# Kernel optimization log

Hardware: AMD Instinct MI355X
Metric: run time of the kernel (lower is better)

Reference implementation:

```python
import jax, jax.numpy as jnp
import numpy as np

B, T, D = 4, 2048, 1024
H = 16
HD = D // H  # 64
MAX_POS = 4096


def setup_inputs() -> dict:
    key = jax.random.key(0)
    k1, k2, k3, k4 = jax.random.split(key, 4)
    x = jax.random.normal(k1, (B, T, D), dtype=jnp.float32)
    position_ids = jnp.sort(jax.random.randint(k2, (B, T), 0, MAX_POS), axis=-1)
    Wqkv = jax.random.normal(k3, (D, 3 * D), dtype=jnp.float32) * (D ** -0.5)
    Wout = jax.random.normal(k4, (D, D), dtype=jnp.float32) * (D ** -0.5)
    return {"x": x, "position_ids": position_ids, "Wqkv": Wqkv, "Wout": Wout}


def reference(x, position_ids, Wqkv, Wout):
    Bv, Tv, Dv = x.shape
    # qkv projection: (B,T,3,H,HD)
    qkv = (x @ Wqkv).reshape(Bv, Tv, 3, H, HD)
    q, k, v = jnp.moveaxis(qkv, 2, 0)  # each (B,T,H,HD)
    q = q.transpose(0, 2, 1, 3)  # (B,H,T,HD)
    k = k.transpose(0, 2, 1, 3)
    v = v.transpose(0, 2, 1, 3)
    scale = 1.0 / jnp.sqrt(jnp.asarray(HD, dtype=x.dtype))
    attn = jnp.einsum('bhid,bhjd->bhij', q, k) * scale  # (B,H,T,T)
    # position-derived causal mask: attend only where pos_i >= pos_j
    causal_mask = position_ids[:, None, :, None] < position_ids[:, None, None, :]
    attn = jnp.where(causal_mask, -jnp.inf, attn)
    attn = jax.nn.softmax(attn, axis=-1)
    attn = jnp.nan_to_num(attn, nan=0.0)
    out = jnp.einsum('bhij,bhjd->bhid', attn, v)  # (B,H,T,HD)
    out = out.transpose(0, 2, 1, 3).reshape(Bv, Tv, Dv)
    return out @ Wout
```

## Files before the change

kernel.cpp:

```cpp
#include <hip/hip_runtime.h>
#include <math.h>

#define NB 4
#define NT 2048
#define ND 1024
#define NH 16
#define NHD 64
#define N3D 3072
#define M1 8192

typedef __attribute__((ext_vector_type(8))) short bf16x8;
typedef __attribute__((ext_vector_type(4))) float f32x4;
typedef __attribute__((ext_vector_type(16))) float f32x16;
typedef __attribute__((ext_vector_type(2))) int i32x2;
typedef unsigned short u16;
typedef unsigned int u32;

#define MNEG -3.0e38f

__device__ __forceinline__ u32 bf16rn(float f) {
    u32 u = __float_as_uint(f);
    return (u + 0x7FFFu + ((u >> 16) & 1u)) >> 16;
}
__device__ __forceinline__ u32 pack2(float a, float b) {
    return bf16rn(a) | (bf16rn(b) << 16);
}
__device__ __forceinline__ u32 cvtpk(float lo, float hi) {
    u32 r;
    asm("v_cvt_pk_bf16_f32 %0, %1, %2" : "=v"(r) : "v"(lo), "v"(hi));
    return r;
}
__device__ __forceinline__ void pswap(u32& a, u32& b) {
    i32x2 r = __builtin_amdgcn_permlane32_swap((int)a, (int)b, false, false);
    a = (u32)r.x; b = (u32)r.y;
}

__global__ __launch_bounds__(256) void bnd_kernel(const int* __restrict__ pos, int* __restrict__ Bnd) {
    const int row = blockIdx.x * 256 + threadIdx.x;
    const int b = row >> 11, i = row & 2047;
    const int target = pos[b * 2048 + i];
    int lo = 0, hi = 2048;
    #pragma unroll
    for (int it = 0; it < 12; ++it) {
        const int mid = (lo + hi) >> 1;
        if (lo < hi) { if (pos[b * 2048 + mid] <= target) lo = mid + 1; else hi = mid; }
    }
    Bnd[row] = lo;
}

__global__ __launch_bounds__(256) void convx_kernel(const float* __restrict__ in, u16* __restrict__ out) {
    const int idx = blockIdx.x * 256 + threadIdx.x;
    const float4 v = *reinterpret_cast<const float4*>(in + (size_t)idx * 4);
    *reinterpret_cast<uint2*>(out + (size_t)idx * 4) = make_uint2(pack2(v.x, v.y), pack2(v.z, v.w));
}

__global__ __launch_bounds__(256) void tconv_kernel(const float* __restrict__ in, u16* __restrict__ out,
                                                    int R, int C) {
    __shared__ float t[32][33];
    const int bx = blockIdx.x * 32, by = blockIdx.y * 32;
    const int x = threadIdx.x, y0 = threadIdx.y;
    #pragma unroll
    for (int yy = y0; yy < 32; yy += 8) t[yy][x] = in[(size_t)(by + yy) * C + bx + x];
    __syncthreads();
    #pragma unroll
    for (int yy = y0; yy < 32; yy += 8) out[(size_t)(bx + yy) * R + by + x] = (u16)bf16rn(t[x][yy]);
}

#define GEMM_PROLOGUE(Aptr, Btptr)                                                            \
    __shared__ __align__(16) u16 As[4096];                                                    \
    __shared__ __align__(16) u16 Bs[4096];                                                    \
    const int tid = threadIdx.x;                                                              \
    const int lane = tid & 63, wave = tid >> 6;                                               \
    const int wr = wave >> 1, wc = wave & 1;                                                  \
    const int n0 = blockIdx.x * 128, m0 = blockIdx.y * 128;                                   \
    const int c0 = tid, c1 = tid + 256;                                                      \
    const int pA0 = (c0 * 16) ^ ((((c0 * 16) >> 6) & 7) << 4);                                \
    const int pA1 = (c1 * 16) ^ ((((c1 * 16) >> 6) & 7) << 4);                                \
    const u16* gA0 = Aptr + (size_t)(m0 + (c0 >> 2)) * 1024 + (c0 & 3) * 8;                   \
    const u16* gA1 = Aptr + (size_t)(m0 + (c1 >> 2)) * 1024 + (c1 & 3) * 8;                   \
    const u16* gB0 = Btptr + (size_t)(n0 + (c0 >> 2)) * 1024 + (c0 & 3) * 8;                  \
    const u16* gB1 = Btptr + (size_t)(n0 + (c1 >> 2)) * 1024 + (c1 & 3) * 8;                  \
    int offA[4], offB[4];                                                                     \
    {                                                                                         \
        const int kb = (lane >> 4) * 16;                                                      \
        _Pragma("unroll")                                                                     \
        for (int mm = 0; mm < 4; ++mm) {                                                      \
            int row = wr * 64 + mm * 16 + (lane & 15);                                        \
            offA[mm] = (row * 64 + kb) ^ ((row & 7) << 4);                                    \
        }                                                                                     \
        _Pragma("unroll")                                                                     \
        for (int nn = 0; nn < 4; ++nn) {                                                      \
            int row = wc * 64 + nn * 16 + (lane & 15);                                        \
            offB[nn] = (row * 64 + kb) ^ ((row & 7) << 4);                                    \
        }                                                                                     \
    }                                                                                         \
    f32x4 acc[4][4];                                                                          \
    _Pragma("unroll")                                                                         \
    for (int mm = 0; mm < 4; ++mm)                                                            \
        _Pragma("unroll")                                                                     \
        for (int nn = 0; nn < 4; ++nn)                                                        \
            acc[mm][nn] = (f32x4){0.f, 0.f, 0.f, 0.f};                                        \
    uint4 va0 = *(const uint4*)gA0, va1 = *(const uint4*)gA1;                                 \
    uint4 vb0 = *(const uint4*)gB0, vb1 = *(const uint4*)gB1;                                 \
    for (int k0 = 0; k0 < 1024; k0 += 32) {                                                   \
        __syncthreads();                                                                      \
        *(uint4*)((char*)As + pA0) = va0;                                                     \
        *(uint4*)((char*)As + pA1) = va1;                                                     \
        *(uint4*)((char*)Bs + pA0) = vb0;                                                     \
        *(uint4*)((char*)Bs + pA1) = vb1;                                                     \
        __syncthreads();                                                                      \
        if (k0 + 32 < 1024) {                                                                 \
            gA0 += 32; gA1 += 32; gB0 += 32; gB1 += 32;                                       \
            va0 = *(const uint4*)gA0; va1 = *(const uint4*)gA1;                               \
            vb0 = *(const uint4*)gB0; vb1 = *(const uint4*)gB1;                               \
        }                                                                                     \
        bf16x8 aF[4], bF[4];                                                                  \
        _Pragma("unroll")                                                                     \
        for (int mm = 0; mm < 4; ++mm) aF[mm] = *(const bf16x8*)((const char*)As + offA[mm]); \
        _Pragma("unroll")                                                                     \
        for (int nn = 0; nn < 4; ++nn) bF[nn] = *(const bf16x8*)((const char*)Bs + offB[nn]); \
        _Pragma("unroll")                                                                     \
        for (int mm = 0; mm < 4; ++mm)                                                        \
            _Pragma("unroll")                                                                 \
            for (int nn = 0; nn < 4; ++nn)                                                    \
                acc[mm][nn] = __builtin_amdgcn_mfma_f32_16x16x32_bf16(bF[nn], aF[mm],         \
                                                                      acc[mm][nn], 0, 0, 0); \
    }

__global__ __launch_bounds__(256) void gemm_qkv_kernel(
    const u16* __restrict__ A, const u16* __restrict__ Bt,
    u16* __restrict__ Qo, u16* __restrict__ Ko, u16* __restrict__ Vo)
{
    GEMM_PROLOGUE(A, Bt)
    const int col16 = lane & 15, g4 = (lane >> 4) << 2;
    const int nb0 = n0 + wc * 64;
    const int tb0 = m0 + wr * 64;
    const int s  = nb0 >> 10;
    const int hh = (nb0 >> 6) & 15;
    const int t0g = tb0 & 2047;
    const int bh = ((tb0 >> 11) << 4) + hh;
    const float sc = (s == 0) ? 0.18033688011112042f : 1.0f;

    __syncthreads();
    u16* lds = (wave & 1) ? Bs : As;
    for (int round = 0; round < 2; ++round) {
        if ((wave >> 1) == round) {
            if (s < 2) {
                #pragma unroll
                for (int mm = 0; mm < 4; ++mm) {
                    const int tl = mm * 16 + col16;
                    #pragma unroll
                    for (int nn = 0; nn < 4; ++nn) {
                        uint2 w = make_uint2(pack2(acc[mm][nn][0] * sc, acc[mm][nn][1] * sc),
                                             pack2(acc[mm][nn][2] * sc, acc[mm][nn][3] * sc));
                        const int off = (tl * 128 + (nn * 16 + g4) * 2) ^ ((tl & 7) << 4);
                        *reinterpret_cast<uint2*>((char*)lds + off) = w;
                    }
                }
                u16* dst = (s == 0) ? Qo : Ko;
                #pragma unroll
                for (int it = 0; it < 8; ++it) {
                    const int row = it * 8 + (lane >> 3);
                    const int off = (row * 128 + (lane & 7) * 16) ^ ((row & 7) << 4);
                    uint4 v = *reinterpret_cast<const uint4*>((const char*)lds + off);
                    *reinterpret_cast<uint4*>(&dst[((size_t)bh * 2048 + t0g + row) * 64 + (lane & 7) * 8]) = v;
                }
            } else {
                #pragma unroll
                for (int mm = 0; mm < 4; ++mm) {
                    const int tl = mm * 16 + col16;
                    #pragma unroll
                    for (int nn = 0; nn < 4; ++nn) {
                        #pragma unroll
                        for (int r = 0; r < 4; ++r) {
                            const int dl = nn * 16 + g4 + r;
                            const int off = (dl * 128 + tl * 2) ^ ((dl & 7) << 4);
                            *reinterpret_cast<u16*>((char*)lds + off) = (u16)bf16rn(acc[mm][nn][r]);
                        }
                    }
                }
                #pragma unroll
                for (int it = 0; it < 8; ++it) {
                    const int row = it * 8 + (lane >> 3);
                    const int off = (row * 128 + (lane & 7) * 16) ^ ((row & 7) << 4);
                    uint4 v = *reinterpret_cast<const uint4*>((const char*)lds + off);
                    *reinterpret_cast<uint4*>(&Vo[((size_t)bh * 64 + row) * 2048 + t0g + (lane & 7) * 8]) = v;
                }
            }
        }
        __syncthreads();
    }
}

__global__ __launch_bounds__(256) void gemm_out_kernel(
    const u16* __restrict__ A, const u16* __restrict__ Bt, float* __restrict__ C)
{
    GEMM_PROLOGUE(A, Bt)
    const int col16 = lane & 15, g4 = (lane >> 4) << 2;
    __syncthreads();
    char* lds = (char*)((wave & 1) ? Bs : As);
    for (int round = 0; round < 2; ++round) {
        if ((wave >> 1) == round) {
            #pragma unroll
            for (int p = 0; p < 2; ++p) {
                #pragma unroll
                for (int mmh = 0; mmh < 2; ++mmh) {
                    const int mm = p * 2 + mmh;
                    const int rl = mmh * 16 + col16;
                    #pragma unroll
                    for (int nn = 0; nn < 4; ++nn) {
                        const int off = (rl * 256 + (nn * 16 + g4) * 4) ^ ((rl & 7) << 4);
                        *reinterpret_cast<f32x4*>(lds + off) = acc[mm][nn];
                    }
                }
                #pragma unroll
                for (int it = 0; it < 8; ++it) {
                    const int row = it * 4 + (lane >> 4);
                    const int off = (row * 256 + col16 * 16) ^ ((row & 7) << 4);
                    float4 v = *reinterpret_cast<const float4*>((const char*)lds + off);
                    const int mg = m0 + wr * 64 + p * 32 + row;
                    *reinterpret_cast<float4*>(&C[(size_t)mg * 1024 + n0 + wc * 64 + col16 * 4]) = v;
                }
            }
        }
        __syncthreads();
    }
}

__global__ __launch_bounds__(64) void attn6_kernel(
    const u16* __restrict__ Q, const u16* __restrict__ K, const u16* __restrict__ Vt,
    const int* __restrict__ Bnd, u32* __restrict__ Pout)
{
    const int bid = blockIdx.x;
    const int x = bid & 7, wgl = bid >> 3;
    const int bh = x * 8 + (wgl >> 7);
    const int w2 = wgl & 127;
    const int qi = 63 - (w2 >> 1);
    const int c  = w2 & 1;
    const int b = bh >> 4;
    const int lane = threadIdx.x;
    const int col = lane & 31, hi = lane >> 5, hi4 = 4 * hi;
    const int i0 = qi * 32;

    const int bnd = Bnd[b * 2048 + i0 + col];
    int bmax = bnd, bmin = bnd;
    #pragma unroll
    for (int s = 1; s < 32; s <<= 1) {
        bmax = max(bmax, __shfl_xor(bmax, s));
        bmin = min(bmin, __shfl_xor(bmin, s));
    }
    const int ntiles = (bmax + 31) >> 5;
    const int halfk  = ((ntiles + 1) >> 1) << 5;
    const int kLo = c ? halfk : 0;
    const int kHi = c ? bmax : min(halfk, bmax);

    const size_t kvrow = (size_t)bh * 2048;
    const size_t vrow  = (size_t)bh * 64;

    bf16x8 qf[4];
    #pragma unroll
    for (int ds = 0; ds < 4; ++ds)
        qf[ds] = *(const bf16x8*)&Q[(kvrow + i0 + col) * 64 + ds * 16 + hi * 8];

    float mrun = MNEG, lrun = 0.f;
    f32x16 oT0, oT1;
    #pragma unroll
    for (int i = 0; i < 16; ++i) { oT0[i] = 0.f; oT1[i] = 0.f; }

    for (int j0 = kLo; j0 < kHi; j0 += 32) {
        bf16x8 kf[4], vfa[2], vfb[2];
        #pragma unroll
        for (int ds = 0; ds < 4; ++ds)
            kf[ds] = *(const bf16x8*)&K[(kvrow + j0 + col) * 64 + ds * 16 + hi * 8];
        #pragma unroll
        for (int kh = 0; kh < 2; ++kh) {
            vfa[kh] = *(const bf16x8*)&Vt[(vrow + col) * 2048 + j0 + kh * 16 + hi * 8];
            vfb[kh] = *(const bf16x8*)&Vt[(vrow + 32 + col) * 2048 + j0 + kh * 16 + hi * 8];
        }

        f32x16 st;
        #pragma unroll
        for (int i = 0; i < 16; ++i) st[i] = 0.f;
        #pragma unroll
        for (int ds = 0; ds < 4; ++ds)
            st = __builtin_amdgcn_mfma_f32_32x32x16_bf16(kf[ds], qf[ds], st, 0, 0, 0);

        if (j0 + 32 > bmin) {
            #pragma unroll
            for (int r = 0; r < 16; ++r) {
                const int kg = j0 + ((r & 3) + 8 * (r >> 2)) + hi4;
                if (kg >= bnd) st[r] = -INFINITY;
            }
        }

        float rm = st[0];
        #pragma unroll
        for (int r = 1; r < 16; ++r) rm = fmaxf(rm, st[r]);
        rm = fmaxf(rm, __shfl_xor(rm, 32));
        if (__any(rm > mrun)) {
            const float mnew = fmaxf(mrun, rm);
            const float factor = __builtin_amdgcn_exp2f(mrun - mnew);
            mrun = mnew;
            lrun *= factor;
            #pragma unroll
            for (int i = 0; i < 16; ++i) { oT0[i] *= factor; oT1[i] *= factor; }
        }
        float psum = 0.f;
        #pragma unroll
        for (int r = 0; r < 16; ++r) {
            const float p = __builtin_amdgcn_exp2f(st[r] - mrun);
            st[r] = p;
            psum += p;
        }
        psum += __shfl_xor(psum, 32);
        lrun += psum;

        u32 W[8];
        #pragma unroll
        for (int r = 0; r < 8; ++r) W[r] = cvtpk(st[2 * r], st[2 * r + 1]);
        u32 a0 = W[0], b0 = W[2]; pswap(a0, b0);
        u32 a1 = W[1], b1 = W[3]; pswap(a1, b1);
        u32 a2 = W[4], b2 = W[6]; pswap(a2, b2);
        u32 a3 = W[5], b3 = W[7]; pswap(a3, b3);
        union { u32 w[4]; bf16x8 v; } p0, p1;
        p0.w[0] = a0; p0.w[1] = a1; p0.w[2] = b0; p0.w[3] = b1;
        p1.w[0] = a2; p1.w[1] = a3; p1.w[2] = b2; p1.w[3] = b3;

        oT0 = __builtin_amdgcn_mfma_f32_32x32x16_bf16(vfa[0], p0.v, oT0, 0, 0, 0);
        oT0 = __builtin_amdgcn_mfma_f32_32x32x16_bf16(vfa[1], p1.v, oT0, 0, 0, 0);
        oT1 = __builtin_amdgcn_mfma_f32_32x32x16_bf16(vfb[0], p0.v, oT1, 0, 0, 0);
        oT1 = __builtin_amdgcn_mfma_f32_32x32x16_bf16(vfb[1], p1.v, oT1, 0, 0, 0);
    }

    const int slot = ((bh << 6) + qi) * 2 + c;
    u32* P = Pout + (size_t)slot * 1152 + lane;
    #pragma unroll
    for (int w = 0; w < 8; ++w) P[w * 64] = cvtpk(oT0[2 * w], oT0[2 * w + 1]);
    #pragma unroll
    for (int w = 0; w < 8; ++w) P[(8 + w) * 64] = cvtpk(oT1[2 * w], oT1[2 * w + 1]);
    P[16 * 64] = __float_as_uint(mrun);
    P[17 * 64] = __float_as_uint(lrun);
}

__global__ __launch_bounds__(64) void attn_combine_kernel(
    const u32* __restrict__ P, u16* __restrict__ AO)
{
    const int t = blockIdx.x;
    const int bh = t >> 6, qi = t & 63;
    const int b = bh >> 4, h = bh & 15;
    const int lane = threadIdx.x;
    const int col = lane & 31, hi4 = 4 * (lane >> 5);
    const u32* A  = P + (size_t)(t * 2) * 1152 + lane;
    const u32* Bp = A + 1152;
    const float mA = __uint_as_float(A[16 * 64]),  lA = __uint_as_float(A[17 * 64]);
    const float mB = __uint_as_float(Bp[16 * 64]), lB = __uint_as_float(Bp[17 * 64]);
    const float mN = fmaxf(mA, mB);
    const float fA = __builtin_amdgcn_exp2f(mA - mN);
    const float fB = __builtin_amdgcn_exp2f(mB - mN);
    const float inv = 1.f / (lA * fA + lB * fB);
    u16* dst = &AO[((size_t)(b * 2048 + qi * 32 + col)) * 1024 + h * 64];
    #pragma unroll
    for (int w = 0; w < 16; ++w) {
        const u32 wa = A[w * 64], wb = Bp[w * 64];
        const float a0 = __uint_as_float(wa << 16), a1 = __uint_as_float(wa & 0xFFFF0000u);
        const float b0 = __uint_as_float(wb << 16), b1 = __uint_as_float(wb & 0xFFFF0000u);
        const float o0 = (a0 * fA + b0 * fB) * inv;
        const float o1 = (a1 * fA + b1 * fB) * inv;
        const int wl = w & 7;
        const int dloc = 8 * (wl >> 1) + 2 * (wl & 1) + hi4 + ((w >> 3) << 5);
        *reinterpret_cast<u32*>(&dst[dloc]) = cvtpk(o0, o1);
    }
}

extern "C" void kernel_launch(void* const* d_in, const int* in_sizes, int n_in,
                              void* d_out, int out_size, void* d_ws, size_t ws_size,
                              hipStream_t stream) {
    (void)in_sizes; (void)n_in; (void)out_size; (void)ws_size;
    const float* x    = (const float*)d_in[0];
    const int*   pos  = (const int*)d_in[1];
    const float* Wqkv = (const float*)d_in[2];
    const float* Wout = (const float*)d_in[3];
    float* out = (float*)d_out;

    char* ws = (char*)d_ws;
    u16* xb    = (u16*)(ws);
    u16* WqkvT = (u16*)(ws + 16777216);
    u16* WoutT = (u16*)(ws + 23068672);
    u16* Qb    = (u16*)(ws + 25165824);
    u16* Kb    = (u16*)(ws + 41943040);
    u16* Vtb   = (u16*)(ws + 58720256);
    u32* Part  = (u32*)(ws + 75497472);
    int* Bnd   = (int*)(ws + 113246208);
    u16* AO    = xb;

    bnd_kernel<<<dim3(M1 / 256), dim3(256), 0, stream>>>(pos, Bnd);
    convx_kernel<<<dim3(M1 * ND / (256 * 4)), dim3(256), 0, stream>>>(x, xb);
    tconv_kernel<<<dim3(N3D / 32, ND / 32), dim3(32, 8), 0, stream>>>(Wqkv, WqkvT, ND, N3D);
    tconv_kernel<<<dim3(ND / 32, ND / 32), dim3(32, 8), 0, stream>>>(Wout, WoutT, ND, ND);
    gemm_qkv_kernel<<<dim3(N3D / 128, M1 / 128), dim3(256), 0, stream>>>(xb, WqkvT, Qb, Kb, Vtb);
    attn6_kernel<<<dim3(8192), dim3(64), 0, stream>>>(Qb, Kb, Vtb, Bnd, Part);
    attn_combine_kernel<<<dim3(4096), dim3(64), 0, stream>>>(Part, AO);
    gemm_out_kernel<<<dim3(ND / 128, M1 / 128), dim3(256), 0, stream>>>(AO, WoutT, out);
}
```

Before: 387.2 us.

## Simplify GEMM epilogues, add V transpose kernel, pack attention waves per block

New measurement: 381.8 us. No clear change (-1.4%).

```diff
diff --git a/kernel.cpp b/kernel.cpp
--- a/kernel.cpp
+++ b/kernel.cpp
@@ -66,6 +66,19 @@
     for (int yy = y0; yy < 32; yy += 8) out[(size_t)(bx + yy) * R + by + x] = (u16)bf16rn(t[x][yy]);
 }
 
+__global__ __launch_bounds__(256) void vtrans_kernel(const u16* __restrict__ in, u16* __restrict__ out) {
+    __shared__ u16 t[32][34];
+    const int dx = blockIdx.x * 32, ty0 = blockIdx.y * 32, bh = blockIdx.z;
+    const int x = threadIdx.x, y0 = threadIdx.y;
+    const u16* src = in + ((size_t)bh * 2048 + ty0) * 64 + dx;
+    #pragma unroll
+    for (int yy = y0; yy < 32; yy += 8) t[yy][x] = src[yy * 64 + x];
+    __syncthreads();
+    u16* dst = out + ((size_t)bh * 64 + dx) * 2048 + ty0;
+    #pragma unroll
+    for (int yy = y0; yy < 32; yy += 8) dst[(size_t)yy * 2048 + x] = t[x][yy];
+}
+
 #define GEMM_PROLOGUE(Aptr, Btptr)                                                            \
     __shared__ __align__(16) u16 As[4096];                                                    \
     __shared__ __align__(16) u16 Bs[4096];                                                    \
@@ -73,7 +86,7 @@
     const int lane = tid & 63, wave = tid >> 6;                                               \
     const int wr = wave >> 1, wc = wave & 1;                                                  \
     const int n0 = blockIdx.x * 128, m0 = blockIdx.y * 128;                                   \
-    const int c0 = tid, c1 = tid + 256;                                                      \
+    const int c0 = tid, c1 = tid + 256;                                                       \
     const int pA0 = (c0 * 16) ^ ((((c0 * 16) >> 6) & 7) << 4);                                \
     const int pA1 = (c1 * 16) ^ ((((c1 * 16) >> 6) & 7) << 4);                                \
     const u16* gA0 = Aptr + (size_t)(m0 + (c0 >> 2)) * 1024 + (c0 & 3) * 8;                   \
@@ -98,7 +111,7 @@
     _Pragma("unroll")                                                                         \
     for (int mm = 0; mm < 4; ++mm)                                                            \
         _Pragma("unroll")                                                                     \
-        for (int nn = 0; nn < 4; ++nn)                                                        \
+        for (int nn = 0; nn < 4; ++nn)                                                       \
             acc[mm][nn] = (f32x4){0.f, 0.f, 0.f, 0.f};                                        \
     uint4 va0 = *(const uint4*)gA0, va1 = *(const uint4*)gA1;                                 \
     uint4 vb0 = *(const uint4*)gB0, vb1 = *(const uint4*)gB1;                                 \
@@ -123,7 +136,7 @@
         for (int mm = 0; mm < 4; ++mm)                                                        \
             _Pragma("unroll")                                                                 \
             for (int nn = 0; nn < 4; ++nn)                                                    \
-                acc[mm][nn] = __builtin_amdgcn_mfma_f32_16x16x32_bf16(bF[nn], aF[mm],         \
+                acc[mm][nn] = __builtin_amdgcn_mfma_f32_16x16x32_bf16(aF[mm], bF[nn],         \
                                                                       acc[mm][nn], 0, 0, 0); \
     }
 
@@ -132,63 +145,23 @@
     u16* __restrict__ Qo, u16* __restrict__ Ko, u16* __restrict__ Vo)
 {
     GEMM_PROLOGUE(A, Bt)
-    const int col16 = lane & 15, g4 = (lane >> 4) << 2;
-    const int nb0 = n0 + wc * 64;
-    const int tb0 = m0 + wr * 64;
-    const int s  = nb0 >> 10;
-    const int hh = (nb0 >> 6) & 15;
-    const int t0g = tb0 & 2047;
-    const int bh = ((tb0 >> 11) << 4) + hh;
+    const int nbase = n0 + wc * 64;
+    const int s  = nbase >> 10;
+    const int hh = (nbase >> 6) & 15;
+    u16* dst = (s == 0) ? Qo : (s == 1) ? Ko : Vo;
     const float sc = (s == 0) ? 0.18033688011112042f : 1.0f;
-
-    __syncthreads();
-    u16* lds = (wave & 1) ? Bs : As;
-    for (int round = 0; round < 2; ++round) {
-        if ((wave >> 1) == round) {
-            if (s < 2) {
-                #pragma unroll
-                for (int mm = 0; mm < 4; ++mm) {
-                    const int tl = mm * 16 + col16;
-                    #pragma unroll
-                    for (int nn = 0; nn < 4; ++nn) {
-                        uint2 w = make_uint2(pack2(acc[mm][nn][0] * sc, acc[mm][nn][1] * sc),
-                                             pack2(acc[mm][nn][2] * sc, acc[mm][nn][3] * sc));
-                        const int off = (tl * 128 + (nn * 16 + g4) * 2) ^ ((tl & 7) << 4);
-                        *reinterpret_cast<uint2*>((char*)lds + off) = w;
-                    }
-                }
-                u16* dst = (s == 0) ? Qo : Ko;
-                #pragma unroll
-                for (int it = 0; it < 8; ++it) {
-                    const int row = it * 8 + (lane >> 3);
-                    const int off = (row * 128 + (lane & 7) * 16) ^ ((row & 7) << 4);
-                    uint4 v = *reinterpret_cast<const uint4*>((const char*)lds + off);
-                    *reinterpret_cast<uint4*>(&dst[((size_t)bh * 2048 + t0g + row) * 64 + (lane & 7) * 8]) = v;
-                }
-            } else {
-                #pragma unroll
-                for (int mm = 0; mm < 4; ++mm) {
-                    const int tl = mm * 16 + col16;
-                    #pragma unroll
-                    for (int nn = 0; nn < 4; ++nn) {
-                        #pragma unroll
-                        for (int r = 0; r < 4; ++r) {
-                            const int dl = nn * 16 + g4 + r;
-                            const int off = (dl * 128 + tl * 2) ^ ((dl & 7) << 4);
-                            *reinterpret_cast<u16*>((char*)lds + off) = (u16)bf16rn(acc[mm][nn][r]);
-                        }
-                    }
-                }
-                #pragma unroll
-                for (int it = 0; it < 8; ++it) {
-                    const int row = it * 8 + (lane >> 3);
-                    const int off = (row * 128 + (lane & 7) * 16) ^ ((row & 7) << 4);
-                    uint4 v = *reinterpret_cast<const uint4*>((const char*)lds + off);
-                    *reinterpret_cast<uint4*>(&Vo[((size_t)bh * 64 + row) * 2048 + t0g + (lane & 7) * 8]) = v;
-                }
-            }
-        }
-        __syncthreads();
+    #pragma unroll
+    for (int nn = 0; nn < 4; ++nn) {
+        const int hd = nn * 16 + (lane & 15);
+        #pragma unroll
+        for (int mm = 0; mm < 4; ++mm) {
+            const int rbase = m0 + wr * 64 + mm * 16 + ((lane >> 4) << 2);
+            const int bq = rbase >> 11, t0 = rbase & 2047;
+            const size_t base = ((size_t)((bq << 4) + hh) * 2048 + t0) * 64 + hd;
+            #pragma unroll
+            for (int r = 0; r < 4; ++r)
+                dst[base + (size_t)r * 64] = (u16)bf16rn(acc[mm][nn][r] * sc);
+        }
     }
 }
 
@@ -196,49 +169,31 @@
     const u16* __restrict__ A, const u16* __restrict__ Bt, float* __restrict__ C)
 {
     GEMM_PROLOGUE(A, Bt)
-    const int col16 = lane & 15, g4 = (lane >> 4) << 2;
-    __syncthreads();
-    char* lds = (char*)((wave & 1) ? Bs : As);
-    for (int round = 0; round < 2; ++round) {
-        if ((wave >> 1) == round) {
+    #pragma unroll
+    for (int nn = 0; nn < 4; ++nn) {
+        const int n_abs = n0 + wc * 64 + nn * 16 + (lane & 15);
+        #pragma unroll
+        for (int mm = 0; mm < 4; ++mm) {
+            const int rbase = m0 + wr * 64 + mm * 16 + ((lane >> 4) << 2);
             #pragma unroll
-            for (int p = 0; p < 2; ++p) {
-                #pragma unroll
-                for (int mmh = 0; mmh < 2; ++mmh) {
-                    const int mm = p * 2 + mmh;
-                    const int rl = mmh * 16 + col16;
-                    #pragma unroll
-                    for (int nn = 0; nn < 4; ++nn) {
-                        const int off = (rl * 256 + (nn * 16 + g4) * 4) ^ ((rl & 7) << 4);
-                        *reinterpret_cast<f32x4*>(lds + off) = acc[mm][nn];
-                    }
-                }
-                #pragma unroll
-                for (int it = 0; it < 8; ++it) {
-                    const int row = it * 4 + (lane >> 4);
-                    const int off = (row * 256 + col16 * 16) ^ ((row & 7) << 4);
-                    float4 v = *reinterpret_cast<const float4*>((const char*)lds + off);
-                    const int mg = m0 + wr * 64 + p * 32 + row;
-                    *reinterpret_cast<float4*>(&C[(size_t)mg * 1024 + n0 + wc * 64 + col16 * 4]) = v;
-                }
-            }
-        }
-        __syncthreads();
-    }
-}
-
-__global__ __launch_bounds__(64) void attn6_kernel(
+            for (int r = 0; r < 4; ++r)
+                C[(size_t)(rbase + r) * 1024 + n_abs] = acc[mm][nn][r];
+        }
+    }
+}
+
+__global__ __launch_bounds__(256, 4) void attn7_kernel(
     const u16* __restrict__ Q, const u16* __restrict__ K, const u16* __restrict__ Vt,
     const int* __restrict__ Bnd, u32* __restrict__ Pout)
 {
+    const int tid = threadIdx.x, lane = tid & 63, wave = tid >> 6;
     const int bid = blockIdx.x;
-    const int x = bid & 7, wgl = bid >> 3;
-    const int bh = x * 8 + (wgl >> 7);
-    const int w2 = wgl & 127;
-    const int qi = 63 - (w2 >> 1);
-    const int c  = w2 & 1;
+    const int x = bid & 7, bl = bid >> 3;
+    const int bh = x * 8 + (bl >> 5);
+    const int u  = (bl & 31) * 4 + wave;
+    const int qi = 63 - (u >> 1);
+    const int c  = u & 1;
     const int b = bh >> 4;
-    const int lane = threadIdx.x;
     const int col = lane & 31, hi = lane >> 5, hi4 = 4 * hi;
     const int i0 = qi * 32;
 
@@ -267,11 +222,13 @@
     #pragma unroll
     for (int i = 0; i < 16; ++i) { oT0[i] = 0.f; oT1[i] = 0.f; }
 
+    bf16x8 kf[4];
+    #pragma unroll
+    for (int ds = 0; ds < 4; ++ds)
+        kf[ds] = *(const bf16x8*)&K[(kvrow + kLo + col) * 64 + ds * 16 + hi * 8];
+
     for (int j0 = kLo; j0 < kHi; j0 += 32) {
-        bf16x8 kf[4], vfa[2], vfb[2];
-        #pragma unroll
-        for (int ds = 0; ds < 4; ++ds)
-            kf[ds] = *(const bf16x8*)&K[(kvrow + j0 + col) * 64 + ds * 16 + hi * 8];
+        bf16x8 vfa[2], vfb[2];
         #pragma unroll
         for (int kh = 0; kh < 2; ++kh) {
             vfa[kh] = *(const bf16x8*)&Vt[(vrow + col) * 2048 + j0 + kh * 16 + hi * 8];
@@ -281,9 +238,17 @@
         f32x16 st;
         #pragma unroll
         for (int i = 0; i < 16; ++i) st[i] = 0.f;
+        __builtin_amdgcn_s_setprio(1);
         #pragma unroll
         for (int ds = 0; ds < 4; ++ds)
             st = __builtin_amdgcn_mfma_f32_32x32x16_bf16(kf[ds], qf[ds], st, 0, 0, 0);
+        __builtin_amdgcn_s_setprio(0);
+
+        const int jn = (j0 + 32 < kHi) ? j0 + 32 : j0;
+        bf16x8 kf2[4];
+        #pragma unroll
+        for (int ds = 0; ds < 4; ++ds)
+            kf2[ds] = *(const bf16x8*)&K[(kvrow + jn + col) * 64 + ds * 16 + hi * 8];
 
         if (j0 + 32 > bmin) {
             #pragma unroll
@@ -326,10 +291,15 @@
         p0.w[0] = a0; p0.w[1] = a1; p0.w[2] = b0; p0.w[3] = b1;
         p1.w[0] = a2; p1.w[1] = a3; p1.w[2] = b2; p1.w[3] = b3;
 
+        __builtin_amdgcn_s_setprio(1);
         oT0 = __builtin_amdgcn_mfma_f32_32x32x16_bf16(vfa[0], p0.v, oT0, 0, 0, 0);
         oT0 = __builtin_amdgcn_mfma_f32_32x32x16_bf16(vfa[1], p1.v, oT0, 0, 0, 0);
         oT1 = __builtin_amdgcn_mfma_f32_32x32x16_bf16(vfb[0], p0.v, oT1, 0, 0, 0);
         oT1 = __builtin_amdgcn_mfma_f32_32x32x16_bf16(vfb[1], p1.v, oT1, 0, 0, 0);
+        __builtin_amdgcn_s_setprio(0);
+
+        #pragma unroll
+        for (int ds = 0; ds < 4; ++ds) kf[ds] = kf2[ds];
     }
 
     const int slot = ((bh << 6) + qi) * 2 + c;
@@ -342,13 +312,13 @@
     P[17 * 64] = __float_as_uint(lrun);
 }
 
-__global__ __launch_bounds__(64) void attn_combine_kernel(
+__global__ __launch_bounds__(256) void attn_combine_kernel(
     const u32* __restrict__ P, u16* __restrict__ AO)
 {
-    const int t = blockIdx.x;
+    const int tid = threadIdx.x, lane = tid & 63, wave = tid >> 6;
+    const int t = blockIdx.x * 4 + wave;
     const int bh = t >> 6, qi = t & 63;
     const int b = bh >> 4, h = bh & 15;
-    const int lane = threadIdx.x;
     const int col = lane & 31, hi4 = 4 * (lane >> 5);
     const u32* A  = P + (size_t)(t * 2) * 1152 + lane;
     const u32* Bp = A + 1152;
@@ -389,6 +359,7 @@
     u16* Qb    = (u16*)(ws + 25165824);
     u16* Kb    = (u16*)(ws + 41943040);
     u16* Vtb   = (u16*)(ws + 58720256);
+    u16* Vb    = (u16*)(ws + 75497472);
     u32* Part  = (u32*)(ws + 75497472);
     int* Bnd   = (int*)(ws + 113246208);
     u16* AO    = xb;
@@ -397,8 +368,9 @@
     convx_kernel<<<dim3(M1 * ND / (256 * 4)), dim3(256), 0, stream>>>(x, xb);
     tconv_kernel<<<dim3(N3D / 32, ND / 32), dim3(32, 8), 0, stream>>>(Wqkv, WqkvT, ND, N3D);
     tconv_kernel<<<dim3(ND / 32, ND / 32), dim3(32, 8), 0, stream>>>(Wout, WoutT, ND, ND);
-    gemm_qkv_kernel<<<dim3(N3D / 128, M1 / 128), dim3(256), 0, stream>>>(xb, WqkvT, Qb, Kb, Vtb);
-    attn6_kernel<<<dim3(8192), dim3(64), 0, stream>>>(Qb, Kb, Vtb, Bnd, Part);
-    attn_combine_kernel<<<dim3(4096), dim3(64), 0, stream>>>(Part, AO);
+    gemm_qkv_kernel<<<dim3(N3D / 128, M1 / 128), dim3(256), 0, stream>>>(xb, WqkvT, Qb, Kb, Vb);
+    vtrans_kernel<<<dim3(2, 64, 64), dim3(32, 8), 0, stream>>>(Vb, Vtb);
+    attn7_kernel<<<dim3(2048), dim3(256), 0, stream>>>(Qb, Kb, Vtb, Bnd, Part);
+    attn_combine_kernel<<<dim3(1024), dim3(256), 0, stream>>>(Part, AO);
     gemm_out_kernel<<<dim3(ND / 128, M1 / 128), dim3(256), 0, stream>>>(AO, WoutT, out);
 }
```
